# Optimization experiments

Hardware: AMD Instinct MI355X
Metric: run time of the kernel (lower is better)

The kernel has to match this reference:

```python
import jax, jax.numpy as jnp
import numpy as np

D = H = W = 64
N = D * H * W
BS = 2
C = 32          # enc_dim
IN_DIM = 4
OUT_DIM = 4
P = 5           # pos_enc_dim
COND = 32
M = 8           # modes per axis
NL = 4          # n_layers
NODE_IN = IN_DIM + 3 + 2 * P * 3   # 37
ENC_T = 1 + 2 * P                  # 11
ENC_C = ENC_T * COND               # 352
DT = 0.05


def fourier_embedding(pos, n_freq):
    # F(x) = [cos(2^i*pi*x_l), sin(2^i*pi*x_l)] per coordinate l, then concat x
    freq = (2.0 ** jnp.arange(n_freq, dtype=jnp.float32)) * jnp.pi  # (P,)
    ang = pos[..., None] * freq                                     # (..., L, P)
    emb = jnp.concatenate([jnp.cos(ang), jnp.sin(ang)], axis=-1)    # (..., L, 2P)
    emb = emb.reshape(*pos.shape[:-1], -1)                          # (..., L*2P)
    return jnp.concatenate([emb, pos], axis=-1)


def setup_inputs() -> dict:
    key = jax.random.key(0)
    ks = jax.random.split(key, 24)
    scale = 1.0 / C ** 2
    inp = {
        "state_in": jax.random.normal(ks[0], (BS, N, IN_DIM), jnp.float32),
        "node_pos": jax.random.uniform(ks[1], (BS, N, 3), jnp.float32),
        "edges": jax.random.randint(ks[2], (BS, 16, 2), 0, N),
        "time_i": jax.random.uniform(ks[3], (BS, 1), jnp.float32),
        "conditions": jax.random.uniform(ks[4], (BS, COND), jnp.float32),
        "t_embed_w": jax.random.normal(ks[5], (C, ENC_T), jnp.float32) * 0.05,
        "t_embed_b": jax.random.normal(ks[6], (C,), jnp.float32) * 0.05,
        "c_embed_w": jax.random.normal(ks[7], (C, ENC_C), jnp.float32) * 0.05,
        "c_embed_b": jax.random.normal(ks[8], (C,), jnp.float32) * 0.05,
        "lift_w": jax.random.normal(ks[9], (C, NODE_IN), jnp.float32) * 0.05,
        "lift_b": jax.random.normal(ks[10], (C,), jnp.float32) * 0.05,
        "spec_wr": jax.random.uniform(ks[11], (NL, C, C, M, M, M), jnp.float32) * scale,
        "spec_wi": jax.random.uniform(ks[12], (NL, C, C, M, M, M), jnp.float32) * scale,
        "byp_w": jax.random.normal(ks[13], (NL, C, C), jnp.float32) * 0.05,
        "byp_b": jax.random.normal(ks[14], (NL, C), jnp.float32) * 0.05,
        "proj1_w": jax.random.normal(ks[15], (C, C), jnp.float32) * 0.05,
        "proj1_b": jax.random.normal(ks[16], (C,), jnp.float32) * 0.05,
        "proj2_w": jax.random.normal(ks[17], (OUT_DIM, C), jnp.float32) * 0.05,
        "proj2_b": jax.random.normal(ks[18], (OUT_DIM,), jnp.float32) * 0.05,
    }
    return inp


def _conv1x1(x, w, b):
    # x: (b, c, d, h, w), w: (o, c), b: (o,)
    return jnp.einsum('bcdhw,oc->bodhw', x, w) + b[None, :, None, None, None]


def _fno_forward(state_in, node_pos, time_i, conditions,
                 t_embed_w, t_embed_b, c_embed_w, c_embed_b, lift_w, lift_b,
                 spec_wr, spec_wi, byp_w, byp_b, proj1_w, proj1_b, proj2_w, proj2_b):
    pos_enc = fourier_embedding(node_pos, P)      # (bs, N, 33)
    c_enc = fourier_embedding(conditions, P)      # (bs, 352)
    t_enc = fourier_embedding(time_i, P)          # (bs, 11)

    node_feat = jnp.concatenate([state_in, pos_enc], axis=-1)  # (bs, N, 37)
    t_emb = (t_enc @ t_embed_w.T + t_embed_b)[:, :, None, None, None]
    c_emb = (c_enc @ c_embed_w.T + c_embed_b)[:, :, None, None, None]

    # (bs, N, 37) -> (bs, 37, D, H, W)
    x = node_feat.transpose(0, 2, 1).reshape(BS, NODE_IN, D, H, W)
    x = _conv1x1(x, lift_w, lift_b)
    x = x + t_emb + c_emb

    for l in range(NL):
        w = jax.lax.complex(spec_wr[l], spec_wi[l])              # (C, C, M, M, M)
        x_ft = jnp.fft.rfftn(x, axes=(-3, -2, -1))               # (bs, C, D, H, W//2+1)
        blk = jnp.einsum('bixyz,ioxyz->boxyz', x_ft[..., :M, :M, :M], w)
        out_ft = jnp.zeros_like(x_ft).at[..., :M, :M, :M].set(blk)
        sp = jnp.fft.irfftn(out_ft, s=(D, H, W), axes=(-3, -2, -1))
        bp = _conv1x1(x, byp_w[l], byp_b[l])
        x = jax.nn.gelu(sp + bp, approximate=False)

    x = jax.nn.gelu(_conv1x1(x, proj1_w, proj1_b), approximate=False)
    x = _conv1x1(x, proj2_w, proj2_b)                            # (bs, 4, D, H, W)
    v_pred = x.reshape(BS, OUT_DIM, N).transpose(0, 2, 1)        # (bs, N, 4)
    return state_in + DT * v_pred


def reference(state_in, node_pos, edges, time_i, conditions,
              t_embed_w, t_embed_b, c_embed_w, c_embed_b, lift_w, lift_b,
              spec_wr, spec_wi, byp_w, byp_b, proj1_w, proj1_b, proj2_w, proj2_b):
    # edges are unused in the FNO forward (kept for API compatibility)
    return _fno_forward(state_in, node_pos, time_i, conditions,
                        t_embed_w, t_embed_b, c_embed_w, c_embed_b, lift_w, lift_b,
                        spec_wr, spec_wi, byp_w, byp_b, proj1_w, proj1_b, proj2_w, proj2_b)
```

## Files before the change

kernel.cpp:

```cpp
#include <hip/hip_runtime.h>
#include <math.h>

#define PI_F 3.14159265358979323846f

typedef __bf16 bf16x8 __attribute__((ext_vector_type(8)));
typedef float floatx4 __attribute__((ext_vector_type(4)));
union U8 { unsigned short u[8]; uint4 q; bf16x8 v; };

__device__ __forceinline__ float gelu_sig(float v) {
    float e = __builtin_amdgcn_exp2f(-2.4554670f * v);
    return v * __builtin_amdgcn_rcpf(1.0f + e);
}
__device__ __forceinline__ int rfl(int x) { return __builtin_amdgcn_readfirstlane(x); }

__device__ __forceinline__ unsigned short f2bf(float f) {
    unsigned int u = __float_as_uint(f);
    u += 0x7fffu + ((u >> 16) & 1u);
    return (unsigned short)(u >> 16);
}
__device__ __forceinline__ float bf2f(unsigned short h) {
    return __uint_as_float(((unsigned int)h) << 16);
}

__global__ void k_emb(const float* __restrict__ time_i, const float* __restrict__ conditions,
                      const float* __restrict__ t_embed_w, const float* __restrict__ t_embed_b,
                      const float* __restrict__ c_embed_w, const float* __restrict__ c_embed_b,
                      const float* __restrict__ lift_b, float* __restrict__ embk) {
    __shared__ float red[8][32];
    int t = threadIdx.x;
    int b = blockIdx.x;
    int c = t & 31, lg = t >> 5;
    float acc = 0.0f;
    if (lg == 0) {
        acc = t_embed_b[c] + c_embed_b[c] + lift_b[c];
        float tv = time_i[b];
        float ang = PI_F * tv;
        const float* tw = t_embed_w + c * 11;
        for (int i = 0; i < 5; i++) {
            float s, co; sincosf(ang, &s, &co);
            acc += co * tw[i] + s * tw[5 + i];
            ang *= 2.0f;
        }
        acc += tv * tw[10];
    }
    const float* cw = c_embed_w + c * 352;
    for (int j = 0; j < 4; j++) {
        int l = lg * 4 + j;
        float v = conditions[b * 32 + l];
        float ang = PI_F * v;
        for (int i = 0; i < 5; i++) {
            float s, co; sincosf(ang, &s, &co);
            acc += co * cw[l * 10 + i] + s * cw[l * 10 + 5 + i];
            ang *= 2.0f;
        }
        acc += v * cw[320 + l];
    }
    red[lg][c] = acc;
    __syncthreads();
    if (t < 32) {
        float s = 0.0f;
        for (int g = 0; g < 8; g++) s += red[g][t];
        embk[b * 32 + t] = s;
    }
}

__global__ void k_wt(const float* __restrict__ byp_w, const float* __restrict__ lift_w,
                     unsigned short* __restrict__ wbh, unsigned short* __restrict__ wlbf,
                     unsigned short* __restrict__ Tinv, unsigned short* __restrict__ TfT,
                     float* __restrict__ Tp1g) {
    int idx = blockIdx.x * 256 + threadIdx.x;
    const float th = PI_F / 32.0f;
    if (idx < 4096) {
        wbh[idx] = f2bf(byp_w[idx]);
    } else if (idx < 6144) {
        int j = idx - 4096;
        int o = j >> 6, q = j & 63;
        wlbf[j] = (q < 37) ? f2bf(lift_w[o * 37 + q]) : 0;
    } else if (idx < 8192) {
        int j = idx - 6144;
        int nz = j >> 5, k = j & 31;
        int kz = k >> 1;
        float val = 0.0f;
        if (kz < 8) {
            float a = (float)((kz * nz) & 63) * th;
            val = (k & 1) ? sinf(a) : cosf(a);
            val *= (kz == 0) ? (1.0f / 262144.0f) : (2.0f / 262144.0f);
        }
        Tinv[j] = f2bf(val);
    } else if (idx < 9216) {
        int j = idx - 8192;
        int kcol = j >> 6, nz = j & 63;
        int kz = kcol >> 1;
        float a = (float)((kz * nz) & 63) * th;
        float val = (kcol & 1) ? -sinf(a) : cosf(a);
        TfT[j] = f2bf(val);
    } else if (idx < 9728) {
        int j = idx - 9216;
        int ny = j >> 3, ky = j & 7;
        float a = (float)((ky * ny) & 63) * th;
        Tp1g[j * 2] = cosf(a);
        Tp1g[j * 2 + 1] = sinf(a);
    }
}

__device__ __forceinline__ void swz8k(int blk, int& b, int& nx, int& ny) {
    int x = blk & 7;
    int j = blk >> 3;
    int pair = x * 16 + (j >> 6);
    ny = j & 63;
    b = pair >> 6;
    nx = pair & 63;
}

__global__ __launch_bounds__(256) void k_lift(const float* __restrict__ state_in,
        const float* __restrict__ node_pos, const unsigned short* __restrict__ wlbf,
        const float* __restrict__ embk, const unsigned short* __restrict__ TfT,
        unsigned short* __restrict__ x0, float2* __restrict__ a1) {
    __shared__ __align__(16) float SL[5024];
    unsigned short* fsT  = (unsigned short*)SL;
    unsigned short* ysbf = (unsigned short*)(SL + 2304);
    float* pz   = SL + 3456;
    float* pz2  = SL + 4480;
    float* bias = SL + 4992;
    int t = threadIdx.x;
    int b, nx, ny; swz8k(blockIdx.x, b, nx, ny);
    int nxy = nx * 64 + ny;

    if (t < 32) bias[t] = embk[b * 32 + t];
    {
        for (int u = t; u < 2048; u += 256) {
            int row = u >> 5, col = 37 + (u & 31);
            fsT[row * 72 + col] = 0;
        }
    }
    if (t < 192) {
        int nzf = t / 3;
        int l = t - nzf * 3;
        float p = node_pos[((size_t)b * 262144 + (nxy << 6)) * 3 + t];
        float s, c; sincosf(PI_F * p, &s, &c);
        unsigned short* row = fsT + nzf * 72;
        #pragma unroll
        for (int i = 0; i < 5; i++) {
            row[4 + l * 10 + i] = f2bf(c);
            row[4 + l * 10 + 5 + i] = f2bf(s);
            float nc = 2.0f * c * c - 1.0f;
            s = 2.0f * s * c;
            c = nc;
        }
        row[34 + l] = f2bf(p);
    } else {
        int nzf = t - 192;
        const float4 s4 = *(const float4*)(state_in + ((size_t)b * 262144 + (nxy << 6) + nzf) * 4);
        unsigned short* row = fsT + nzf * 72;
        row[0] = f2bf(s4.x); row[1] = f2bf(s4.y);
        row[2] = f2bf(s4.z); row[3] = f2bf(s4.w);
    }
    __syncthreads();

    int lane = t & 63;
    int w = rfl(t >> 6);
    int otile = w & 1;
    int nzt0 = (w >> 1) * 2;
    int l15 = lane & 15;
    int quad = lane >> 4;

    U8 a0, a1_;
    a0.q = *(const uint4*)(wlbf + ((otile * 16 + l15) << 6) + (quad << 3));
    a1_.q = *(const uint4*)(wlbf + ((otile * 16 + l15) << 6) + 32 + (quad << 3));
    floatx4 cb;
    #pragma unroll
    for (int r = 0; r < 4; r++) cb[r] = bias[otile * 16 + quad * 4 + r];
    floatx4 dz = {0.0f, 0.0f, 0.0f, 0.0f};

    #pragma unroll
    for (int m = 0; m < 2; m++) {
        int nzc = (nzt0 + m) * 16 + l15;
        U8 b0, b1_;
        b0.q = *(const uint4*)(fsT + nzc * 72 + (quad << 3));
        b1_.q = *(const uint4*)(fsT + nzc * 72 + 32 + (quad << 3));
        floatx4 d = __builtin_amdgcn_mfma_f32_16x16x32_bf16(a0.v, b0.v, cb, 0, 0, 0);
        d = __builtin_amdgcn_mfma_f32_16x16x32_bf16(a1_.v, b1_.v, d, 0, 0, 0);
        #pragma unroll
        for (int r = 0; r < 4; r++) {
            int o = otile * 16 + quad * 4 + r;
            ysbf[o * 72 + nzc] = f2bf(d[r]);
        }
    }
    __syncthreads();
    {
        int ch = t >> 3, q = t & 7;
        uint4 v = *(const uint4*)(ysbf + ch * 72 + q * 8);
        *(uint4*)(x0 + (((size_t)(b * 32 + ch)) << 18) + (nxy << 6) + q * 8) = v;
    }
    {
        int khalf = w >> 1;
        U8 ay, bt;
        ay.q = *(const uint4*)(ysbf + (otile * 16 + l15) * 72 + khalf * 32 + (quad << 3));
        bt.q = *(const uint4*)(TfT + (l15 << 6) + khalf * 32 + (quad << 3));
        floatx4 d = __builtin_amdgcn_mfma_f32_16x16x32_bf16(ay.v, bt.v, dz, 0, 0, 0);
        *(floatx4*)(pz + w * 256 + lane * 4) = d;
    }
    __syncthreads();
    if (w < 2) {
        float4 p0 = *(float4*)(pz + w * 256 + lane * 4);
        float4 p1 = *(float4*)(pz + (w + 2) * 256 + lane * 4);
        float pv[4] = {p0.x + p1.x, p0.y + p1.y, p0.z + p1.z, p0.w + p1.w};
        #pragma unroll
        for (int r = 0; r < 4; r++)
            pz2[(otile * 16 + quad * 4 + r) * 16 + l15] = pv[r];
    }
    __syncthreads();
    if (t < 128) {
        float4 v = *(float4*)(pz2 + t * 4);
        float* a1f = (float*)a1 + ((size_t)(b * 4096 + nxy)) * 512;
        *(float4*)(a1f + t * 4) = v;
    }
}


__global__ __launch_bounds__(256) void k_p1(const float2* __restrict__ a1,
        const float2* __restrict__ Tp1g, float2* __restrict__ a2p) {
    int blk = blockIdx.x, t = threadIdx.x;
    int x = blk & 7, r = blk >> 3;
    int pair = x * 16 + (r & 15);
    int qtr = r >> 4;
    const float2* src = a1 + ((size_t)(pair * 64 + qtr * 16)) * 256 + t;
    float accr[8], acci[8];
    #pragma unroll
    for (int k = 0; k < 8; k++) { accr[k] = 0.0f; acci[k] = 0.0f; }
    #pragma unroll 4
    for (int j = 0; j < 16; j++) {
        int ny = qtr * 16 + j;
        float2 v = src[(size_t)j * 256];
        const float2* tw = Tp1g + ny * 8;
        #pragma unroll
        for (int ky = 0; ky < 8; ky++) {
            float2 w2 = tw[ky];
            accr[ky] += v.x * w2.x + v.y * w2.y;
            acci[ky] += v.y * w2.x - v.x * w2.y;
        }
    }
    float4* dst = (float4*)(a2p + (size_t)qtr * 262144 + ((size_t)(pair * 256 + t)) * 8);
    #pragma unroll
    for (int j = 0; j < 4; j++)
        dst[j] = make_float4(accr[2 * j], acci[2 * j], accr[2 * j + 1], acci[2 * j + 1]);
}

__global__ __launch_bounds__(256) void k_p2(const float2* __restrict__ a2p,
                                            float2* __restrict__ xft) {
    __shared__ __align__(16) float2 SH[1040];
    int blk = blockIdx.x, t = threadIdx.x;
    for (int lu = 0; lu < 2; lu++) {
        int un = blk * 2 + lu;
        int b = un >> 8, ckz = un & 255;
        size_t base = (size_t)b * 131072 + (size_t)ckz * 8;
        for (int e = t; e < 512; e += 256) {
            size_t a = base + (size_t)(e >> 3) * 2048 + (e & 7);
            float2 v0 = a2p[a];
            float2 v1 = a2p[a + 262144];
            float2 v2 = a2p[a + 524288];
            float2 v3 = a2p[a + 786432];
            SH[lu * 520 + e] = make_float2(v0.x + v1.x + v2.x + v3.x,
                                           v0.y + v1.y + v2.y + v3.y);
        }
    }
    __syncthreads();
    if (t < 128) {
        int lu = t >> 6, out = t & 63;
        int un = blk * 2 + lu;
        int kx = out & 7;
        float sn, cc; sincosf((float)kx * (PI_F / 32.0f), &sn, &cc);
        float bsn = -sn;
        float tc = 1.0f, ts = 0.0f, rr = 0.0f, ri = 0.0f;
        const float2* row = SH + lu * 520 + (out >> 3);
        for (int nx = 0; nx < 64; nx++) {
            float2 v = row[nx * 8];
            rr += v.x * tc - v.y * ts;
            ri += v.x * ts + v.y * tc;
            float nt = tc * cc - ts * bsn; ts = ts * cc + tc * bsn; tc = nt;
        }
        xft[(size_t)un * 64 + out] = make_float2(rr, ri);
    }
}

__global__ __launch_bounds__(256) void k_p3(const float2* __restrict__ xft,
        const float* __restrict__ wr, const float* __restrict__ wi,
        float2* __restrict__ yftp) {
    __shared__ __align__(16) float2 SH[64];
    int blk = blockIdx.x, t = threadIdx.x;
    int unit = blk >> 2, iq = blk & 3;
    int b = unit >> 6, kx = (unit >> 3) & 7, ky = unit & 7;
    if (t < 64) {
        int il = t >> 3, kz = t & 7;
        int i = iq * 8 + il;
        SH[t] = xft[((size_t)((b * 32 + i) * 8 + kz)) * 64 + ky * 8 + kx];
    }
    __syncthreads();
    int o = t >> 3, kz = t & 7;
    float yr = 0.0f, yi = 0.0f;
    for (int il = 0; il < 8; il++) {
        int i = iq * 8 + il;
        float2 xv = SH[il * 8 + kz];
        int wofs = ((i * 32 + o) << 9) + kx * 64 + ky * 8 + kz;
        float wrv = wr[wofs], wiv = wi[wofs];
        yr += xv.x * wrv - xv.y * wiv;
        yi += xv.x * wiv + xv.y * wrv;
    }
    yftp[(size_t)iq * 32768 + ((size_t)((b * 32 + o) * 8 + kz)) * 64 + ky * 8 + kx]
        = make_float2(yr, yi);
}

__global__ __launch_bounds__(256) void k_p4(const float2* __restrict__ yftp,
                                            float2* __restrict__ b1) {
    __shared__ __align__(16) float2 SH[4608];
    int blk = blockIdx.x, t = threadIdx.x;
    for (int u = 0; u < 2; u++) {
        if (u) __syncthreads();
        int unit = blk * 2 + u;
        int b = unit >> 8, nx = (unit >> 2) & 63, og = unit & 3;
        size_t sbase = ((size_t)(b * 32 + og * 8)) * 512;
        for (int e = t; e < 4096; e += 256) {
            float2 v0 = yftp[sbase + e];
            float2 v1 = yftp[32768 + sbase + e];
            float2 v2 = yftp[65536 + sbase + e];
            float2 v3 = yftp[98304 + sbase + e];
            SH[(e >> 3) * 9 + (e & 7)] = make_float2(v0.x + v1.x + v2.x + v3.x,
                                                     v0.y + v1.y + v2.y + v3.y);
        }
        __syncthreads();
        float cs, ss; sincosf((float)nx * (PI_F / 32.0f), &ss, &cs);
        float2* dst = b1 + ((size_t)(b * 64 + nx)) * 2048 + og * 512;
        for (int h = 0; h < 2; h++) {
            int idx = h * 256 + t;
            const float2* row = SH + idx * 9;
            float c = 1.0f, s = 0.0f, rr = 0.0f, ri = 0.0f;
            #pragma unroll
            for (int kx = 0; kx < 8; kx++) {
                float2 y = row[kx];
                rr += y.x * c - y.y * s;
                ri += y.x * s + y.y * c;
                float nc = c * cs - s * ss; s = s * cs + c * ss; c = nc;
            }
            dst[idx] = make_float2(rr, ri);
        }
    }
}

__global__ __launch_bounds__(256) void k_fin(
        const unsigned short* __restrict__ xin, const float2* __restrict__ b1,
        const unsigned short* __restrict__ wbh, const float* __restrict__ bb,
        const unsigned short* __restrict__ Tinv, const unsigned short* __restrict__ TfT,
        const float2* __restrict__ Tp1g, unsigned short* __restrict__ xout,
        float2* __restrict__ a1, int do_z, int do_proj,
        const float* __restrict__ state_in, const float* __restrict__ p1w,
        const float* __restrict__ p1b, const float* __restrict__ p2w,
        const float* __restrict__ p2b, float* __restrict__ outp) {
    __shared__ __align__(16) float S[4416];
    float* pz   = S;
    float* pz2  = S + 1024;
    float* pr   = S;
    unsigned short* xsu  = (unsigned short*)(S + 1536);
    unsigned short* msbf = (unsigned short*)(S + 2592);
    unsigned short* ysbf = (unsigned short*)(S + 3232);
    float* bias = S + 4384;
    int t = threadIdx.x;
    int b, nx, ny; swz8k(blockIdx.x, b, nx, ny);
    int nxy = nx * 64 + ny;

    if (t >= 96 && t < 128) bias[t - 96] = bb[t - 96];
    ((unsigned int*)msbf)[(t >> 3) * 20 + 8 + (t & 7)] = 0;
    {
        int ch = t >> 3, q = t & 7;
        uint4 v = *(const uint4*)(xin + (((size_t)b) << 23) + (nxy << 6)
                                  + ((size_t)ch << 18) + q * 8);
        unsigned int* dst = (unsigned int*)(xsu + ch * 66 + q * 8);
        dst[0] = v.x; dst[1] = v.y; dst[2] = v.z; dst[3] = v.w;
    }
    {
        const float4* g = (const float4*)(b1 + ((size_t)(b * 64 + nx)) * 2048
                                          + (size_t)t * 8);
        float4 g0 = g[0], g1 = g[1], g2 = g[2], g3 = g[3];
        float vr[8], vi[8];
        vr[0] = g0.x; vi[0] = g0.y; vr[1] = g0.z; vi[1] = g0.w;
        vr[2] = g1.x; vi[2] = g1.y; vr[3] = g1.z; vi[3] = g1.w;
        vr[4] = g2.x; vi[4] = g2.y; vr[5] = g2.z; vi[5] = g2.w;
        vr[6] = g3.x; vi[6] = g3.y; vr[7] = g3.z; vi[7] = g3.w;
        const float2* tw = Tp1g + ny * 8;
        float mr = 0.0f, mi = 0.0f;
        #pragma unroll
        for (int ky = 0; ky < 8; ky++) {
            float2 w2 = tw[ky];
            mr += vr[ky] * w2.x - vi[ky] * w2.y;
            mi += vr[ky] * w2.y + vi[ky] * w2.x;
        }
        unsigned int pk = (unsigned int)f2bf(mr)
                        | ((unsigned int)f2bf(-mi) << 16);
        ((unsigned int*)msbf)[(t >> 3) * 20 + (t & 7)] = pk;
    }
    __syncthreads();

    int lane = t & 63;
    int w = rfl(t >> 6);
    int otile = w & 1;
    int nzt0 = (w >> 1) * 2;
    int l15 = lane & 15;
    int quad = lane >> 4;

    U8 aw, ams;
    aw.q = *(const uint4*)(wbh + ((otile * 16 + l15) << 5) + (quad << 3));
    ams.q = *(const uint4*)(msbf + (otile * 16 + l15) * 40 + (quad << 3));
    floatx4 cb;
    #pragma unroll
    for (int r = 0; r < 4; r++) cb[r] = bias[otile * 16 + quad * 4 + r];
    floatx4 dzero = {0.0f, 0.0f, 0.0f, 0.0f};

    size_t colbase = (((size_t)b) << 23) + (nxy << 6);

    #pragma unroll
    for (int m = 0; m < 2; m++) {
        int nzc = (nzt0 + m) * 16 + l15;
        U8 bx, bt;
        #pragma unroll
        for (int j = 0; j < 8; j++) bx.u[j] = xsu[(quad * 8 + j) * 66 + nzc];
        bt.q = *(const uint4*)(Tinv + (nzc << 5) + (quad << 3));
        floatx4 d = __builtin_amdgcn_mfma_f32_16x16x32_bf16(aw.v, bx.v, cb, 0, 0, 0);
        d = __builtin_amdgcn_mfma_f32_16x16x32_bf16(ams.v, bt.v, d, 0, 0, 0);
        #pragma unroll
        for (int r = 0; r < 4; r++) {
            int o = otile * 16 + quad * 4 + r;
            ysbf[o * 72 + nzc] = f2bf(gelu_sig(d[r]));
        }
    }
    __syncthreads();

    if (!do_proj) {
        int ch = t >> 3, q = t & 7;
        uint4 v = *(const uint4*)(ysbf + ch * 72 + q * 8);
        *(uint4*)(xout + colbase + ((size_t)ch << 18) + q * 8) = v;
    }

    if (do_z) {
        int khalf = w >> 1;
        U8 ay, bt;
        ay.q = *(const uint4*)(ysbf + (otile * 16 + l15) * 72 + khalf * 32 + (quad << 3));
        bt.q = *(const uint4*)(TfT + (l15 << 6) + khalf * 32 + (quad << 3));
        floatx4 d = __builtin_amdgcn_mfma_f32_16x16x32_bf16(ay.v, bt.v, dzero, 0, 0, 0);
        *(floatx4*)(pz + w * 256 + lane * 4) = d;
        __syncthreads();
        if (w < 2) {
            float4 p0 = *(float4*)(pz + w * 256 + lane * 4);
            float4 p1 = *(float4*)(pz + (w + 2) * 256 + lane * 4);
            float pv[4] = {p0.x + p1.x, p0.y + p1.y, p0.z + p1.z, p0.w + p1.w};
            #pragma unroll
            for (int r = 0; r < 4; r++)
                pz2[(otile * 16 + quad * 4 + r) * 16 + l15] = pv[r];
        }
        __syncthreads();
        if (t < 128) {
            float4 v = *(float4*)(pz2 + t * 4);
            float* a1f = (float*)a1 + ((size_t)(b * 4096 + nxy)) * 512;
            *(float4*)(a1f + t * 4) = v;
        }
    }

    if (do_proj) {
        int nz = t & 63;
        float xv[32];
        #pragma unroll
        for (int i = 0; i < 32; i++) xv[i] = bf2f(ysbf[i * 72 + nz]);
        float r0 = 0.f, r1 = 0.f, r2 = 0.f, r3 = 0.f;
        #pragma unroll
        for (int k = 0; k < 8; k++) {
            int o = w * 8 + k;
            float a = p1b[o];
            const float* wr = p1w + o * 32;
            #pragma unroll
            for (int i = 0; i < 32; i++) a += wr[i] * xv[i];
            float h = gelu_sig(a);
            r0 += p2w[0 * 32 + o] * h;
            r1 += p2w[1 * 32 + o] * h;
            r2 += p2w[2 * 32 + o] * h;
            r3 += p2w[3 * 32 + o] * h;
        }
        *(float4*)(pr + w * 256 + nz * 4) = make_float4(r0, r1, r2, r3);
        __syncthreads();
        if (t < 64) {
            float4 a0 = *(float4*)(pr + 0 * 256 + t * 4);
            float4 a1_ = *(float4*)(pr + 1 * 256 + t * 4);
            float4 a2 = *(float4*)(pr + 2 * 256 + t * 4);
            float4 a3 = *(float4*)(pr + 3 * 256 + t * 4);
            size_t base = ((size_t)b * 262144 + (nxy << 6) + t) * 4;
            float4 sv = *(const float4*)(state_in + base);
            *(float4*)(outp + base) = make_float4(
                sv.x + 0.05f * (p2b[0] + a0.x + a1_.x + a2.x + a3.x),
                sv.y + 0.05f * (p2b[1] + a0.y + a1_.y + a2.y + a3.y),
                sv.z + 0.05f * (p2b[2] + a0.z + a1_.z + a2.z + a3.z),
                sv.w + 0.05f * (p2b[3] + a0.w + a1_.w + a2.w + a3.w));
        }
    }
}

extern "C" void kernel_launch(void* const* d_in, const int* in_sizes, int n_in,
                              void* d_out, int out_size, void* d_ws, size_t ws_size,
                              hipStream_t stream) {
    const float* state_in   = (const float*)d_in[0];
    const float* node_pos   = (const float*)d_in[1];
    const float* time_i     = (const float*)d_in[3];
    const float* conditions = (const float*)d_in[4];
    const float* t_embed_w  = (const float*)d_in[5];
    const float* t_embed_b  = (const float*)d_in[6];
    const float* c_embed_w  = (const float*)d_in[7];
    const float* c_embed_b  = (const float*)d_in[8];
    const float* lift_w     = (const float*)d_in[9];
    const float* lift_b     = (const float*)d_in[10];
    const float* spec_wr    = (const float*)d_in[11];
    const float* spec_wi    = (const float*)d_in[12];
    const float* byp_w      = (const float*)d_in[13];
    const float* byp_b      = (const float*)d_in[14];
    const float* proj1_w    = (const float*)d_in[15];
    const float* proj1_b    = (const float*)d_in[16];
    const float* proj2_w    = (const float*)d_in[17];
    const float* proj2_b    = (const float*)d_in[18];
    float* out = (float*)d_out;
    float* ws  = (float*)d_ws;

    unsigned short* xA = (unsigned short*)ws;
    unsigned short* xB = (unsigned short*)(ws + 8388608);
    float2* a1   = (float2*)(ws + 16777216);
    float2* a2p  = (float2*)(ws + 20971520);
    float2* xft  = (float2*)(ws + 23068672);
    float2* yftp = (float2*)(ws + 23134208);
    float2* b1   = (float2*)(ws + 23396352);
    float*  embk = ws + 23920640;
    unsigned short* wbh  = (unsigned short*)(ws + 23920704);
    unsigned short* wlbf = (unsigned short*)(ws + 23922752);
    unsigned short* Tinv = (unsigned short*)(ws + 23923776);
    unsigned short* TfT  = (unsigned short*)(ws + 23924800);
    float* Tp1gf = ws + 23925312;
    float2* Tp1g = (float2*)Tp1gf;

    k_emb<<<2, 256, 0, stream>>>(time_i, conditions, t_embed_w, t_embed_b,
                                 c_embed_w, c_embed_b, lift_b, embk);
    k_wt<<<38, 256, 0, stream>>>(byp_w, lift_w, wbh, wlbf, Tinv, TfT, Tp1gf);
    k_lift<<<8192, 256, 0, stream>>>(state_in, node_pos, wlbf, embk, TfT, xA, a1);

    for (int l = 0; l < 4; l++) {
        unsigned short* xin  = (l & 1) ? xB : xA;
        unsigned short* xout = (l & 1) ? xA : xB;
        const float* wrl = spec_wr + (size_t)l * 524288;
        const float* wil = spec_wi + (size_t)l * 524288;
        k_p1<<<512, 256, 0, stream>>>(a1, Tp1g, a2p);
        k_p2<<<256, 256, 0, stream>>>(a2p, xft);
        k_p3<<<512, 256, 0, stream>>>(xft, wrl, wil, yftp);
        k_p4<<<256, 256, 0, stream>>>(yftp, b1);
        k_fin<<<8192, 256, 0, stream>>>(xin, b1, wbh + l * 1024, byp_b + l * 32,
                                        Tinv, TfT, Tp1g, xout, a1, (l < 3) ? 1 : 0,
                                        (l == 3) ? 1 : 0, state_in,
                                        proj1_w, proj1_b, proj2_w, proj2_b, out);
    }
}
```

Before: 344.9 us.

## Store z-transformed intermediate a1 in bf16 and merge embedding kernel into setup

Changes the a1 buffer, the partial z-DFT output written by k_lift/k_fin and read by k_p1, from float2 to packed bf16 pairs. This halves that buffer's write and read traffic. It also merges the k_emb launch into k_wt as two extra blocks to save one kernel launch. The cost is lower precision in the spectral path input.

New measurement: 344.5 us. About the same (-0.1%).

```diff
diff --git a/kernel.cpp b/kernel.cpp
--- a/kernel.cpp
+++ b/kernel.cpp
@@ -21,55 +21,59 @@
 __device__ __forceinline__ float bf2f(unsigned short h) {
     return __uint_as_float(((unsigned int)h) << 16);
 }
-
-__global__ void k_emb(const float* __restrict__ time_i, const float* __restrict__ conditions,
-                      const float* __restrict__ t_embed_w, const float* __restrict__ t_embed_b,
-                      const float* __restrict__ c_embed_w, const float* __restrict__ c_embed_b,
-                      const float* __restrict__ lift_b, float* __restrict__ embk) {
-    __shared__ float red[8][32];
-    int t = threadIdx.x;
-    int b = blockIdx.x;
-    int c = t & 31, lg = t >> 5;
-    float acc = 0.0f;
-    if (lg == 0) {
-        acc = t_embed_b[c] + c_embed_b[c] + lift_b[c];
-        float tv = time_i[b];
-        float ang = PI_F * tv;
-        const float* tw = t_embed_w + c * 11;
-        for (int i = 0; i < 5; i++) {
-            float s, co; sincosf(ang, &s, &co);
-            acc += co * tw[i] + s * tw[5 + i];
-            ang *= 2.0f;
-        }
-        acc += tv * tw[10];
-    }
-    const float* cw = c_embed_w + c * 352;
-    for (int j = 0; j < 4; j++) {
-        int l = lg * 4 + j;
-        float v = conditions[b * 32 + l];
-        float ang = PI_F * v;
-        for (int i = 0; i < 5; i++) {
-            float s, co; sincosf(ang, &s, &co);
-            acc += co * cw[l * 10 + i] + s * cw[l * 10 + 5 + i];
-            ang *= 2.0f;
-        }
-        acc += v * cw[320 + l];
-    }
-    red[lg][c] = acc;
-    __syncthreads();
-    if (t < 32) {
-        float s = 0.0f;
-        for (int g = 0; g < 8; g++) s += red[g][t];
-        embk[b * 32 + t] = s;
-    }
-}
-
-__global__ void k_wt(const float* __restrict__ byp_w, const float* __restrict__ lift_w,
+__device__ __forceinline__ unsigned int pack2(float a, float b) {
+    return (unsigned int)f2bf(a) | ((unsigned int)f2bf(b) << 16);
+}
+
+__global__ void k_wt(const float* __restrict__ time_i, const float* __restrict__ conditions,
+                     const float* __restrict__ t_embed_w, const float* __restrict__ t_embed_b,
+                     const float* __restrict__ c_embed_w, const float* __restrict__ c_embed_b,
+                     const float* __restrict__ lift_b, float* __restrict__ embk,
+                     const float* __restrict__ byp_w, const float* __restrict__ lift_w,
                      unsigned short* __restrict__ wbh, unsigned short* __restrict__ wlbf,
                      unsigned short* __restrict__ Tinv, unsigned short* __restrict__ TfT,
                      float* __restrict__ Tp1g) {
-    int idx = blockIdx.x * 256 + threadIdx.x;
     const float th = PI_F / 32.0f;
+    int t = threadIdx.x;
+    if (blockIdx.x < 2) {
+        __shared__ float red[8][32];
+        int b = blockIdx.x;
+        int c = t & 31, lg = t >> 5;
+        float acc = 0.0f;
+        if (lg == 0) {
+            acc = t_embed_b[c] + c_embed_b[c] + lift_b[c];
+            float tv = time_i[b];
+            float ang = PI_F * tv;
+            const float* tw = t_embed_w + c * 11;
+            for (int i = 0; i < 5; i++) {
+                float s, co; sincosf(ang, &s, &co);
+                acc += co * tw[i] + s * tw[5 + i];
+                ang *= 2.0f;
+            }
+            acc += tv * tw[10];
+        }
+        const float* cw = c_embed_w + c * 352;
+        for (int j = 0; j < 4; j++) {
+            int l = lg * 4 + j;
+            float v = conditions[b * 32 + l];
+            float ang = PI_F * v;
+            for (int i = 0; i < 5; i++) {
+                float s, co; sincosf(ang, &s, &co);
+                acc += co * cw[l * 10 + i] + s * cw[l * 10 + 5 + i];
+                ang *= 2.0f;
+            }
+            acc += v * cw[320 + l];
+        }
+        red[lg][c] = acc;
+        __syncthreads();
+        if (t < 32) {
+            float s = 0.0f;
+            for (int g = 0; g < 8; g++) s += red[g][t];
+            embk[b * 32 + t] = s;
+        }
+        return;
+    }
+    int idx = (blockIdx.x - 2) * 256 + t;
     if (idx < 4096) {
         wbh[idx] = f2bf(byp_w[idx]);
     } else if (idx < 6144) {
@@ -115,7 +119,7 @@
 __global__ __launch_bounds__(256) void k_lift(const float* __restrict__ state_in,
         const float* __restrict__ node_pos, const unsigned short* __restrict__ wlbf,
         const float* __restrict__ embk, const unsigned short* __restrict__ TfT,
-        unsigned short* __restrict__ x0, float2* __restrict__ a1) {
+        unsigned short* __restrict__ x0, unsigned int* __restrict__ a1) {
     __shared__ __align__(16) float SL[5024];
     unsigned short* fsT  = (unsigned short*)SL;
     unsigned short* ysbf = (unsigned short*)(SL + 2304);
@@ -212,32 +216,34 @@
     __syncthreads();
     if (t < 128) {
         float4 v = *(float4*)(pz2 + t * 4);
-        float* a1f = (float*)a1 + ((size_t)(b * 4096 + nxy)) * 512;
-        *(float4*)(a1f + t * 4) = v;
-    }
-}
-
-
-__global__ __launch_bounds__(256) void k_p1(const float2* __restrict__ a1,
+        unsigned int* a1p = a1 + ((size_t)(b * 4096 + nxy)) * 256;
+        *(uint2*)(a1p + t * 2) = make_uint2(pack2(v.x, v.y), pack2(v.z, v.w));
+    }
+}
+
+
+__global__ __launch_bounds__(256) void k_p1(const unsigned int* __restrict__ a1,
         const float2* __restrict__ Tp1g, float2* __restrict__ a2p) {
     int blk = blockIdx.x, t = threadIdx.x;
     int x = blk & 7, r = blk >> 3;
     int pair = x * 16 + (r & 15);
     int qtr = r >> 4;
-    const float2* src = a1 + ((size_t)(pair * 64 + qtr * 16)) * 256 + t;
+    const unsigned int* src = a1 + ((size_t)(pair * 64 + qtr * 16)) * 256 + t;
     float accr[8], acci[8];
     #pragma unroll
     for (int k = 0; k < 8; k++) { accr[k] = 0.0f; acci[k] = 0.0f; }
     #pragma unroll 4
     for (int j = 0; j < 16; j++) {
         int ny = qtr * 16 + j;
-        float2 v = src[(size_t)j * 256];
+        unsigned int pv = src[(size_t)j * 256];
+        float vx = bf2f((unsigned short)(pv & 0xffffu));
+        float vy = bf2f((unsigned short)(pv >> 16));
         const float2* tw = Tp1g + ny * 8;
         #pragma unroll
         for (int ky = 0; ky < 8; ky++) {
             float2 w2 = tw[ky];
-            accr[ky] += v.x * w2.x + v.y * w2.y;
-            acci[ky] += v.y * w2.x - v.x * w2.y;
+            accr[ky] += vx * w2.x + vy * w2.y;
+            acci[ky] += vy * w2.x - vx * w2.y;
         }
     }
     float4* dst = (float4*)(a2p + (size_t)qtr * 262144 + ((size_t)(pair * 256 + t)) * 8);
@@ -351,7 +357,7 @@
         const unsigned short* __restrict__ wbh, const float* __restrict__ bb,
         const unsigned short* __restrict__ Tinv, const unsigned short* __restrict__ TfT,
         const float2* __restrict__ Tp1g, unsigned short* __restrict__ xout,
-        float2* __restrict__ a1, int do_z, int do_proj,
+        unsigned int* __restrict__ a1, int do_z, int do_proj,
         const float* __restrict__ state_in, const float* __restrict__ p1w,
         const float* __restrict__ p1b, const float* __restrict__ p2w,
         const float* __restrict__ p2b, float* __restrict__ outp) {
@@ -393,9 +399,7 @@
             mr += vr[ky] * w2.x - vi[ky] * w2.y;
             mi += vr[ky] * w2.y + vi[ky] * w2.x;
         }
-        unsigned int pk = (unsigned int)f2bf(mr)
-                        | ((unsigned int)f2bf(-mi) << 16);
-        ((unsigned int*)msbf)[(t >> 3) * 20 + (t & 7)] = pk;
+        ((unsigned int*)msbf)[(t >> 3) * 20 + (t & 7)] = pack2(mr, -mi);
     }
     __syncthreads();
 
@@ -458,8 +462,8 @@
         __syncthreads();
         if (t < 128) {
             float4 v = *(float4*)(pz2 + t * 4);
-            float* a1f = (float*)a1 + ((size_t)(b * 4096 + nxy)) * 512;
-            *(float4*)(a1f + t * 4) = v;
+            unsigned int* a1p = a1 + ((size_t)(b * 4096 + nxy)) * 256;
+            *(uint2*)(a1p + t * 2) = make_uint2(pack2(v.x, v.y), pack2(v.z, v.w));
         }
     }
 
@@ -526,7 +530,7 @@
 
     unsigned short* xA = (unsigned short*)ws;
     unsigned short* xB = (unsigned short*)(ws + 8388608);
-    float2* a1   = (float2*)(ws + 16777216);
+    unsigned int* a1 = (unsigned int*)(ws + 16777216);
     float2* a2p  = (float2*)(ws + 20971520);
     float2* xft  = (float2*)(ws + 23068672);
     float2* yftp = (float2*)(ws + 23134208);
@@ -539,9 +543,9 @@
     float* Tp1gf = ws + 23925312;
     float2* Tp1g = (float2*)Tp1gf;
 
-    k_emb<<<2, 256, 0, stream>>>(time_i, conditions, t_embed_w, t_embed_b,
-                                 c_embed_w, c_embed_b, lift_b, embk);
-    k_wt<<<38, 256, 0, stream>>>(byp_w, lift_w, wbh, wlbf, Tinv, TfT, Tp1gf);
+    k_wt<<<40, 256, 0, stream>>>(time_i, conditions, t_embed_w, t_embed_b,
+                                 c_embed_w, c_embed_b, lift_b, embk,
+                                 byp_w, lift_w, wbh, wlbf, Tinv, TfT, Tp1gf);
     k_lift<<<8192, 256, 0, stream>>>(state_in, node_pos, wlbf, embk, TfT, xA, a1);
 
     for (int l = 0; l < 4; l++) {
```
